# Kernel tuning notes

Hardware: AMD Instinct MI355X
Metric: run time of the kernel (lower is better)

Reference implementation:

```python
import jax, jax.numpy as jnp
import numpy as np

B, M, D, H = 2, 2048, 1024, 16
DH = D // H            # 64 head dim
FF = 2624              # GeGLU intermediate size
EPS = 1e-5
ROPE_BASE = 10000.0


def _layernorm(x, g, b):
    mu = jnp.mean(x, axis=-1, keepdims=True)
    var = jnp.mean(jnp.square(x - mu), axis=-1, keepdims=True)
    return (x - mu) * jax.lax.rsqrt(var + EPS) * g + b


def _rope_cos_sin(m, dh):
    # HF-style: inv_freq over even dims; only first dh/2 entries are used by apply_rope
    inv_freq = 1.0 / (ROPE_BASE ** (jnp.arange(0, dh, 2, dtype=jnp.float32) / dh))  # [dh/2]
    ang = jnp.arange(m, dtype=jnp.float32)[:, None] * inv_freq[None, :]             # [M, dh/2]
    return jnp.cos(ang), jnp.sin(ang)


def _apply_rope(x, c, s):
    # x: [B,H,M,dh]; c,s: [M,dh/2] broadcast over B,H. Half-split (non-interleaved) rotation.
    x1, x2 = jnp.split(x, 2, axis=-1)
    return jnp.concatenate([x1 * c - x2 * s, x1 * s + x2 * c], axis=-1)


def setup_inputs() -> dict:
    key = jax.random.key(0)
    ks = jax.random.split(key, 6)
    w = lambda k, shape: (jax.random.normal(k, shape, jnp.float32) * 0.02)
    return {
        "hidden_states": jax.random.normal(ks[0], (B, M, D), jnp.float32),
        "attention_mask": jnp.ones((B, M), jnp.int32),
        "ln1_g": jnp.ones((D,), jnp.float32),
        "ln1_b": jnp.zeros((D,), jnp.float32),
        "Wqkv_w": w(ks[1], (3 * D, D)),
        "Wqkv_b": jnp.zeros((3 * D,), jnp.float32),
        "Wo_w": w(ks[2], (D, D)),
        "ln2_g": jnp.ones((D,), jnp.float32),
        "ln2_b": jnp.zeros((D,), jnp.float32),
        "Wi_w": w(ks[3], (2 * FF, D)),
        "Wmlp_o_w": w(ks[4], (D, FF)),
    }


def reference(hidden_states, attention_mask, ln1_g, ln1_b, Wqkv_w, Wqkv_b, Wo_w,
              ln2_g, ln2_b, Wi_w, Wmlp_o_w):
    x = hidden_states                                    # [B,M,D]
    xn = _layernorm(x, ln1_g, ln1_b)
    qkv = xn @ Wqkv_w.T + Wqkv_b                         # [B,M,3D]
    qkv = qkv.reshape(B, M, 3, H, DH).transpose(0, 3, 1, 2, 4)  # [B,H,M,3,dh]
    q, k, v = qkv[..., 0, :], qkv[..., 1, :], qkv[..., 2, :]    # each [B,H,M,dh]

    c, s = _rope_cos_sin(M, DH)                          # [M, dh/2]
    q = _apply_rope(q, c, s)
    k = _apply_rope(k, c, s)

    scale = 1.0 / np.sqrt(DH)
    scores = jnp.einsum("bhmd,bhnd->bhmn", q, k) * scale  # [B,H,M,M]
    keep = (attention_mask > 0)[:, None, None, :]         # [B,1,1,M] padding mask on keys
    scores = jnp.where(keep, scores, -jnp.inf)
    p = jax.nn.softmax(scores, axis=-1)
    o = jnp.einsum("bhmn,bhnd->bhmd", p, v)               # [B,H,M,dh]

    attn_out = o.transpose(0, 2, 1, 3).reshape(B, M, D)
    x = x + attn_out @ Wo_w.T

    # ModernBERT GeGLU MLP: input, gate = Wi(x).chunk(2); Wo(gelu(input) * gate)
    xn2 = _layernorm(x, ln2_g, ln2_b)
    hg = xn2 @ Wi_w.T                                     # [B,M,2*FF]
    h_in, h_gate = jnp.split(hg, 2, axis=-1)
    x = x + (jax.nn.gelu(h_in) * h_gate) @ Wmlp_o_w.T
    return x
```

## Files before the change

kernel.cpp:

```cpp
#include <hip/hip_runtime.h>
#include <cstdint>
#include <cstddef>

using u16 = unsigned short;
using u32 = uint32_t;

typedef __attribute__((ext_vector_type(8))) short short8;
typedef __attribute__((ext_vector_type(4))) float floatx4;
typedef __attribute__((ext_vector_type(4))) unsigned int uintx4;

#define DEVFN static __device__ __forceinline__

#define QSCALE 0.18033688011112042f

DEVFN u16 f2bf(float f) {
  u32 u = __float_as_uint(f);
  return (u16)((u + 0x7fffu + ((u >> 16) & 1u)) >> 16);
}

DEVFN float b2f(u16 u) { return __uint_as_float(((u32)u) << 16); }

DEVFN u32 pkbf(float lo, float hi) {
  return __builtin_amdgcn_perm(__float_as_uint(hi) + 0x8000u,
                               __float_as_uint(lo) + 0x8000u, 0x07060302u);
}

DEVFN void async_load16(const void* g, const void* lds) {
  __builtin_amdgcn_global_load_lds(
      (const __attribute__((address_space(1))) u32*)(uintptr_t)g,
      (__attribute__((address_space(3))) u32*)(u32)(uintptr_t)lds,
      16, 0, 0);
}

DEVFN void cvt4(const float* __restrict__ src, u16* __restrict__ dst, int i) {
  const float4 v = ((const float4*)src)[i];
  ushort4 o;
  o.x = f2bf(v.x); o.y = f2bf(v.y); o.z = f2bf(v.z); o.w = f2bf(v.w);
  ((ushort4*)dst)[i] = o;
}

__global__ __launch_bounds__(256)
void prep_k(const float* __restrict__ Wqkv, const float* __restrict__ Wo,
            const float* __restrict__ Wi, const float* __restrict__ Wmlp,
            const float* __restrict__ hidden, const float* __restrict__ ln1g,
            const float* __restrict__ ln1b,
            u16* __restrict__ wqkv_bf, u16* __restrict__ wo_bf,
            u16* __restrict__ wi_bf, u16* __restrict__ wmlp_bf,
            float* __restrict__ ct, float* __restrict__ st, u16* __restrict__ xn) {
  const int bid = blockIdx.x;
  const int tid = threadIdx.x;
  __shared__ float red[8];
  if (bid < 256) {
    const int i = bid * 256 + tid;
    const int m = i >> 5, f = i & 31;
    const float inv = exp2f((float)f * -0.41524101186092025f);
    const float ang = (float)m * inv;
    ct[i] = cosf(ang);
    st[i] = sinf(ang);
  } else if (bid < 3328) {
    cvt4(Wqkv, wqkv_bf, (bid - 256) * 256 + tid);
  } else if (bid < 4352) {
    cvt4(Wo, wo_bf, (bid - 3328) * 256 + tid);
  } else if (bid < 9600) {
    const int i = (bid - 4352) * 256 + tid;
    const int i4 = i * 4;
    const int p = i4 >> 10, kc = i4 & 1023;
    const int g = p >> 5, c = p & 31;
    const int srow = (c < 16) ? (g * 16 + c) : (2624 + g * 16 + (c - 16));
    const float4 v = *(const float4*)(Wi + (size_t)srow * 1024 + kc);
    ushort4 o;
    o.x = f2bf(v.x); o.y = f2bf(v.y); o.z = f2bf(v.z); o.w = f2bf(v.w);
    ((ushort4*)wi_bf)[i] = o;
  } else if (bid < 12224) {
    cvt4(Wmlp, wmlp_bf, (bid - 9600) * 256 + tid);
  } else {
    const int row = bid - 12224;
    const float4 v = ((const float4*)(hidden + (size_t)row * 1024))[tid];
    float s = v.x + v.y + v.z + v.w;
    float ss = v.x * v.x + v.y * v.y + v.z * v.z + v.w * v.w;
#pragma unroll
    for (int d = 32; d > 0; d >>= 1) {
      s += __shfl_xor(s, d);
      ss += __shfl_xor(ss, d);
    }
    const int wave = tid >> 6;
    if ((tid & 63) == 0) { red[wave] = s; red[4 + wave] = ss; }
    __syncthreads();
    s = red[0] + red[1] + red[2] + red[3];
    ss = red[4] + red[5] + red[6] + red[7];
    const float mu = s * (1.f / 1024.f);
    const float var = ss * (1.f / 1024.f) - mu * mu;
    const float rr = rsqrtf(var + 1e-5f);
    const float4 gv = ((const float4*)ln1g)[tid];
    const float4 bv = ((const float4*)ln1b)[tid];
    u16* orow = xn + (size_t)row * 1024 + tid * 4;
    orow[0] = f2bf((v.x - mu) * rr * gv.x + bv.x);
    orow[1] = f2bf((v.y - mu) * rr * gv.y + bv.y);
    orow[2] = f2bf((v.z - mu) * rr * gv.z + bv.z);
    orow[3] = f2bf((v.w - mu) * rr * gv.w + bv.w);
  }
}

__global__ __launch_bounds__(256)
void red_ln_k(const float* __restrict__ resid, const u16* __restrict__ p0,
              const u16* __restrict__ p1, const u16* __restrict__ p2,
              const float* __restrict__ g, const float* __restrict__ bb,
              float* __restrict__ outx, u16* __restrict__ outn) {
  const int row = blockIdx.x;
  const int tid = threadIdx.x;
  const size_t base = (size_t)row * 1024;
  const float4 h = ((const float4*)(resid + base))[tid];
  const ushort4 a = ((const ushort4*)(p0 + base))[tid];
  const ushort4 c = ((const ushort4*)(p1 + base))[tid];
  const ushort4 d = ((const ushort4*)(p2 + base))[tid];
  float4 v;
  v.x = h.x + b2f(a.x) + b2f(c.x) + b2f(d.x);
  v.y = h.y + b2f(a.y) + b2f(c.y) + b2f(d.y);
  v.z = h.z + b2f(a.z) + b2f(c.z) + b2f(d.z);
  v.w = h.w + b2f(a.w) + b2f(c.w) + b2f(d.w);
  float s = v.x + v.y + v.z + v.w;
  float ss = v.x * v.x + v.y * v.y + v.z * v.z + v.w * v.w;
#pragma unroll
  for (int dd = 32; dd > 0; dd >>= 1) {
    s += __shfl_xor(s, dd);
    ss += __shfl_xor(ss, dd);
  }
  __shared__ float red[8];
  const int wave = tid >> 6;
  if ((tid & 63) == 0) { red[wave] = s; red[4 + wave] = ss; }
  __syncthreads();
  s = red[0] + red[1] + red[2] + red[3];
  ss = red[4] + red[5] + red[6] + red[7];
  const float mu = s * (1.f / 1024.f);
  const float var = ss * (1.f / 1024.f) - mu * mu;
  const float rr = rsqrtf(var + 1e-5f);
  ((float4*)(outx + base))[tid] = v;
  const float4 gv = ((const float4*)g)[tid];
  const float4 bv = ((const float4*)bb)[tid];
  u16* orow = outn + base + tid * 4;
  orow[0] = f2bf((v.x - mu) * rr * gv.x + bv.x);
  orow[1] = f2bf((v.y - mu) * rr * gv.y + bv.y);
  orow[2] = f2bf((v.z - mu) * rr * gv.z + bv.z);
  orow[3] = f2bf((v.w - mu) * rr * gv.w + bv.w);
}

__global__ void red_add_k(float* __restrict__ out, const u16* __restrict__ p0,
                          const u16* __restrict__ p1, const u16* __restrict__ p2,
                          const u16* __restrict__ p3) {
  const int i = blockIdx.x * 256 + threadIdx.x;
  float4 v = ((const float4*)out)[i];
  const ushort4 a = ((const ushort4*)p0)[i];
  const ushort4 c = ((const ushort4*)p1)[i];
  const ushort4 d = ((const ushort4*)p2)[i];
  const ushort4 e = ((const ushort4*)p3)[i];
  v.x += b2f(a.x) + b2f(c.x) + b2f(d.x) + b2f(e.x);
  v.y += b2f(a.y) + b2f(c.y) + b2f(d.y) + b2f(e.y);
  v.z += b2f(a.z) + b2f(c.z) + b2f(d.z) + b2f(e.z);
  v.w += b2f(a.w) + b2f(c.w) + b2f(d.w) + b2f(e.w);
  ((float4*)out)[i] = v;
}

__global__ __launch_bounds__(256)
void red_att_k(u16* __restrict__ att, const u16* __restrict__ p0,
               const float* __restrict__ li0, const float* __restrict__ li1) {
  const int i = blockIdx.x * 256 + threadIdx.x;
  const int i4 = i * 4;
  const int row = i4 >> 10;
  const int col = i4 & 1023;
  const int b = row >> 11, m = row & 2047;
  const int h = col >> 6;
  const int bhm = (b * 16 + h) * 2048 + m;
  const float rl = 1.f / (li0[bhm] + li1[bhm]);
  const ushort4 a = ((const ushort4*)p0)[i];
  const ushort4 c = ((const ushort4*)att)[i];
  ushort4 o;
  o.x = f2bf((b2f(a.x) + b2f(c.x)) * rl);
  o.y = f2bf((b2f(a.y) + b2f(c.y)) * rl);
  o.z = f2bf((b2f(a.z) + b2f(c.z)) * rl);
  o.w = f2bf((b2f(a.w) + b2f(c.w)) * rl);
  ((ushort4*)att)[i] = o;
}

DEVFN void swizzle_tile(int NT, int& tn, int& tm) {
  const int tpx = gridDim.x >> 3;
  const int p = blockIdx.x;
  const int lid = (p & 7) * tpx + (p >> 3);
  const int band = lid / (8 * NT);
  const int rem = lid - band * 8 * NT;
  tn = (rem >> 3) * 128;
  tm = (band * 8 + (rem & 7)) * 128;
}

struct EpiArgs {
  const float* bias;
  u16* q; u16* kk; u16* vt;
  u16* outbf;
  const float* ct; const float* st;
};

template <int EPI>
__global__ __launch_bounds__(256, 3)
void gemm_k(const u16* __restrict__ A, const u16* __restrict__ B, int K, int NT,
            EpiArgs ea) {
  __shared__ __align__(16) u16 sA[128 * 32];
  __shared__ __align__(16) u16 sB[128 * 32];
  int tn, tm;
  swizzle_tile(NT, tn, tm);
  const int tid = threadIdx.x;
  const int wave = tid >> 6, lane = tid & 63;
  const int quad = lane >> 4, l15 = lane & 15;
  const int wm = (wave >> 1) * 64, wn = (wave & 1) * 64;

  floatx4 acc[4][4];
#pragma unroll
  for (int i = 0; i < 4; ++i)
#pragma unroll
    for (int j = 0; j < 4; ++j) acc[i][j] = (floatx4){0.f, 0.f, 0.f, 0.f};

  const int srow = lane >> 2;
  const int skc = (lane & 3) * 8;
  const u16* sAr = sA + (wm + l15) * 32 + quad * 8;
  const u16* sBr = sB + (wn + l15) * 32 + quad * 8;

  for (int k0 = 0; k0 < K; k0 += 32) {
#pragma unroll
    for (int j = 0; j < 2; ++j) {
      const int q = wave * 2 + j;
      const int row = q * 16 + srow;
      async_load16(A + (size_t)(tm + row) * K + (k0 + skc), (const char*)sA + q * 1024);
      async_load16(B + (size_t)(tn + row) * K + (k0 + skc), (const char*)sB + q * 1024);
    }
    __syncthreads();
    short8 af[4], bfr[4];
#pragma unroll
    for (int t = 0; t < 4; ++t) af[t] = *(const short8*)(sAr + t * 512);
#pragma unroll
    for (int t = 0; t < 4; ++t) bfr[t] = *(const short8*)(sBr + t * 512);
#pragma unroll
    for (int ti = 0; ti < 4; ++ti)
#pragma unroll
      for (int tj = 0; tj < 4; ++tj)
        acc[ti][tj] = __builtin_amdgcn_mfma_f32_16x16x32_bf16(af[ti], bfr[tj], acc[ti][tj], 0, 0, 0);
    __syncthreads();
  }

  if constexpr (EPI == 0) {
    const int col0 = tn + wn;
    const int t = col0 >> 10;
    const int h = (col0 & 1023) >> 6;
    if (t == 2) {
#pragma unroll
      for (int ti = 0; ti < 4; ++ti)
#pragma unroll
        for (int r = 0; r < 4; ++r) {
          const int row = tm + wm + ti * 16 + quad * 4 + r;
          const int b = row >> 11, m = row & 2047;
          const int mp = (m & ~31) | ((m & 12) << 1) | ((m & 16) >> 2) | (m & 3);
#pragma unroll
          for (int tj = 0; tj < 4; ++tj) {
            const int dh = tj * 16 + l15;
            const float v = acc[ti][tj][r] + ea.bias[col0 + dh];
            ea.vt[((size_t)((b * 16 + h) * 64 + dh)) * 2048 + mp] = f2bf(v);
          }
        }
    } else {
      u16* dst = (t == 0) ? ea.q : ea.kk;
      const float qs = (t == 0) ? QSCALE : 1.f;
#pragma unroll
      for (int ti = 0; ti < 4; ++ti)
#pragma unroll
        for (int r = 0; r < 4; ++r) {
          const int row = tm + wm + ti * 16 + quad * 4 + r;
          const int b = row >> 11, m = row & 2047;
          u16* drow = dst + ((size_t)(b * 16 + h) * 2048 + m) * 64;
#pragma unroll
          for (int tj = 0; tj < 2; ++tj) {
            const int i = tj * 16 + l15;
            const float x1 = acc[ti][tj][r] + ea.bias[col0 + i];
            const float x2 = acc[ti][tj + 2][r] + ea.bias[col0 + 32 + i];
            const float cs = ea.ct[m * 32 + i];
            const float sn = ea.st[m * 32 + i];
            drow[i] = f2bf((x1 * cs - x2 * sn) * qs);
            drow[32 + i] = f2bf((x1 * sn + x2 * cs) * qs);
          }
        }
    }
  } else {
#pragma unroll
    for (int ti = 0; ti < 4; ++ti)
#pragma unroll
      for (int r = 0; r < 4; ++r) {
        const int row = tm + wm + ti * 16 + quad * 4 + r;
#pragma unroll
        for (int u = 0; u < 2; ++u) {
          const float hin = acc[ti][2 * u][r];
          const float hg = acc[ti][2 * u + 1][r];
          const int a = (((tn + wn) >> 5) + u) * 16 + l15;
          const float t2 = hin + 0.044715f * hin * hin * hin;
          const float e = __builtin_amdgcn_exp2f(t2 * -2.302114768f);
          const float gl = hin * __builtin_amdgcn_rcpf(1.f + e);
          ea.outbf[(size_t)row * 2624 + a] = f2bf(gl * hg);
        }
      }
  }
}

__global__ __launch_bounds__(256, 3)
void gemm_sk4(const u16* __restrict__ A, const u16* __restrict__ B, int K, int NT,
              int kps1, int zsw, int kps2,
              u16* __restrict__ p0, u16* __restrict__ p1,
              u16* __restrict__ p2, u16* __restrict__ p3) {
  __shared__ __align__(16) u16 sA[128 * 32];
  __shared__ __align__(16) u16 sB[128 * 32];
  int tn, tm;
  swizzle_tile(NT, tn, tm);
  const int z = blockIdx.y;
  int kofs, kps;
  if (z < zsw) { kofs = z * kps1; kps = kps1; }
  else { kofs = zsw * kps1 + (z - zsw) * kps2; kps = kps2; }
  const int tid = threadIdx.x;
  const int wave = tid >> 6, lane = tid & 63;
  const int quad = lane >> 4, l15 = lane & 15;
  const int wm = (wave >> 1) * 64, wn = (wave & 1) * 64;

  floatx4 acc[4][4];
#pragma unroll
  for (int i = 0; i < 4; ++i)
#pragma unroll
    for (int j = 0; j < 4; ++j) acc[i][j] = (floatx4){0.f, 0.f, 0.f, 0.f};

  const int srow = lane >> 2;
  const int skc = (lane & 3) * 8;
  const u16* sAr = sA + (wm + l15) * 32 + quad * 8;
  const u16* sBr = sB + (wn + l15) * 32 + quad * 8;

  for (int k0 = 0; k0 < kps; k0 += 32) {
    const int kk = kofs + k0;
#pragma unroll
    for (int j = 0; j < 2; ++j) {
      const int q = wave * 2 + j;
      const int row = q * 16 + srow;
      async_load16(A + (size_t)(tm + row) * K + (kk + skc), (const char*)sA + q * 1024);
      async_load16(B + (size_t)(tn + row) * K + (kk + skc), (const char*)sB + q * 1024);
    }
    __syncthreads();
    short8 af[4], bfr[4];
#pragma unroll
    for (int t = 0; t < 4; ++t) af[t] = *(const short8*)(sAr + t * 512);
#pragma unroll
    for (int t = 0; t < 4; ++t) bfr[t] = *(const short8*)(sBr + t * 512);
#pragma unroll
    for (int ti = 0; ti < 4; ++ti)
#pragma unroll
      for (int tj = 0; tj < 4; ++tj)
        acc[ti][tj] = __builtin_amdgcn_mfma_f32_16x16x32_bf16(af[ti], bfr[tj], acc[ti][tj], 0, 0, 0);
    __syncthreads();
  }

  u16* part = (z == 0) ? p0 : (z == 1) ? p1 : (z == 2) ? p2 : p3;
#pragma unroll
  for (int ti = 0; ti < 4; ++ti)
#pragma unroll
    for (int r = 0; r < 4; ++r) {
      const int row = tm + wm + ti * 16 + quad * 4 + r;
#pragma unroll
      for (int tj = 0; tj < 4; ++tj)
        part[(size_t)row * 1024 + tn + wn + tj * 16 + l15] = f2bf(acc[ti][tj][r]);
    }
}

DEVFN void attn_stage64(const u16* __restrict__ kg, const u16* __restrict__ vtg,
                        size_t bhk, size_t bhv, int key0, int wave, int lane,
                        const u16* sK, const u16* sV) {
#pragma unroll
  for (int j = 0; j < 4; ++j) {
    const int qi = wave * 4 + j;
    if (qi < 8) {
      async_load16(kg + bhk + (size_t)(key0 + lane) * 64 + qi * 8,
                   (const char*)sK + qi * 1024);
    } else {
      const int vi = qi - 8;
      const int c = vi >> 2, kc = vi & 3;
      async_load16(vtg + bhv + (size_t)lane * 2048 + key0 + c * 32 + kc * 8,
                   (const char*)sV + vi * 1024);
    }
  }
}

__global__ __launch_bounds__(256, 3)
void attn_k(const u16* __restrict__ qg, const u16* __restrict__ kg,
            const u16* __restrict__ vtg, const int* __restrict__ mask,
            u16* __restrict__ p0g, u16* __restrict__ p1g,
            float* __restrict__ li0, float* __restrict__ li1) {
  __shared__ __align__(16) u16 sKV[2][8192];
  const int L = blockIdx.x;
  const int xcd = L & 7, idx = L >> 3;
  const int bh = (xcd << 2) | (idx >> 5);
  const int local = idx & 31;
  const int q0 = (local >> 1) * 128;
  const int z = local & 1;
  const int keyBase = z << 10;
  const int b = bh >> 4, h = bh & 15;
  const int tid = threadIdx.x;
  const int wave = tid >> 6, lane = tid & 63;
  const int quad = lane >> 4, l15 = lane & 15;
  const size_t bhk = (size_t)bh * 2048 * 64;
  const size_t bhv = (size_t)bh * 64 * 2048;

  u32 avbits = 0;
#pragma unroll
  for (int kt = 0; kt < 16; ++kt) {
    const bool ok = mask[b * 2048 + keyBase + kt * 64 + lane] > 0;
    if (__all(ok)) avbits |= (1u << kt);
  }

  short8 aq[2][2];
#pragma unroll
  for (int g = 0; g < 2; ++g) {
    const u16* qptr = qg + ((size_t)bh * 2048 + q0 + wave * 32 + g * 16 + l15) * 64 + quad * 8;
    aq[g][0] = *(const short8*)qptr;
    aq[g][1] = *(const short8*)(qptr + 32);
  }

  floatx4 o[2][4];
#pragma unroll
  for (int g = 0; g < 2; ++g)
#pragma unroll
    for (int t = 0; t < 4; ++t) o[g][t] = (floatx4){0.f, 0.f, 0.f, 0.f};
  float li[2] = {0.f, 0.f};
  const floatx4 z4 = {0.f, 0.f, 0.f, 0.f};

  attn_stage64(kg, vtg, bhk, bhv, keyBase, wave, lane, sKV[0], sKV[0] + 4096);
  __syncthreads();

  int buf = 0;
  for (int kt = 0; kt < 16; ++kt) {
    const u16* sK = sKV[buf];
    const u16* sV = sKV[buf] + 4096;
    const int key0 = keyBase + kt * 64;
    if (kt < 15) {
      attn_stage64(kg, vtg, bhk, bhv, key0 + 64, wave, lane,
                   sKV[buf ^ 1], sKV[buf ^ 1] + 4096);
    }
    const bool allv = (avbits >> kt) & 1u;

    short8 pa[2][2];
#pragma unroll
    for (int g = 0; g < 2; ++g) {
      floatx4 sacc[4];
      __builtin_amdgcn_s_setprio(1);
#pragma unroll
      for (int tj = 0; tj < 4; ++tj) {
        const short8 b0 = *(const short8*)(sK + quad * 512 + (tj * 16 + l15) * 8);
        const short8 b1 = *(const short8*)(sK + (4 + quad) * 512 + (tj * 16 + l15) * 8);
        sacc[tj] = __builtin_amdgcn_mfma_f32_16x16x32_bf16(b0, aq[g][0], z4, 0, 0, 0);
        sacc[tj] = __builtin_amdgcn_mfma_f32_16x16x32_bf16(b1, aq[g][1], sacc[tj], 0, 0, 0);
      }
      __builtin_amdgcn_s_setprio(0);

      if (allv) {
        float sum = li[g];
#pragma unroll
        for (int tj = 0; tj < 4; ++tj)
#pragma unroll
          for (int r = 0; r < 4; ++r) {
            const float p = __builtin_amdgcn_exp2f(sacc[tj][r]);
            sacc[tj][r] = p;
            sum += p;
          }
        li[g] = sum;
      } else {
        float sum = li[g];
#pragma unroll
        for (int tj = 0; tj < 4; ++tj)
#pragma unroll
          for (int r = 0; r < 4; ++r) {
            const int key = key0 + tj * 16 + quad * 4 + r;
            const float mb = (mask[b * 2048 + key] > 0) ? 0.f : -1e30f;
            const float p = __builtin_amdgcn_exp2f(sacc[tj][r] + mb);
            sacc[tj][r] = p;
            sum += p;
          }
        li[g] = sum;
      }

#pragma unroll
      for (int c = 0; c < 2; ++c) {
        uintx4 w;
        w.x = pkbf(sacc[2 * c][0], sacc[2 * c][1]);
        w.y = pkbf(sacc[2 * c][2], sacc[2 * c][3]);
        w.z = pkbf(sacc[2 * c + 1][0], sacc[2 * c + 1][1]);
        w.w = pkbf(sacc[2 * c + 1][2], sacc[2 * c + 1][3]);
        pa[g][c] = __builtin_bit_cast(short8, w);
      }
    }

#pragma unroll
    for (int c = 0; c < 2; ++c) {
      __builtin_amdgcn_s_setprio(1);
#pragma unroll
      for (int tj2 = 0; tj2 < 4; ++tj2) {
        const short8 bv = *(const short8*)(sV + (c * 4 + quad) * 512 + (tj2 * 16 + l15) * 8);
        o[0][tj2] = __builtin_amdgcn_mfma_f32_16x16x32_bf16(pa[0][c], bv, o[0][tj2], 0, 0, 0);
        o[1][tj2] = __builtin_amdgcn_mfma_f32_16x16x32_bf16(pa[1][c], bv, o[1][tj2], 0, 0, 0);
      }
      __builtin_amdgcn_s_setprio(0);
    }
    __syncthreads();
    buf ^= 1;
  }

#pragma unroll
  for (int g = 0; g < 2; ++g) {
    float s = li[g];
    s += __shfl_xor(s, 16);
    s += __shfl_xor(s, 32);
    li[g] = s;
  }

  u16* pz = z ? p1g : p0g;
  float* lz = z ? li1 : li0;
  if (lane < 16) {
#pragma unroll
    for (int g = 0; g < 2; ++g)
      lz[(size_t)bh * 2048 + q0 + wave * 32 + g * 16 + l15] = li[g];
  }

#pragma unroll
  for (int g = 0; g < 2; ++g)
#pragma unroll
    for (int tj = 0; tj < 4; ++tj)
#pragma unroll
      for (int r = 0; r < 4; ++r) {
        const int m = q0 + wave * 32 + g * 16 + quad * 4 + r;
        pz[((size_t)b * 2048 + m) * 1024 + h * 64 + tj * 16 + l15] = f2bf(o[g][tj][r]);
      }
}

static const size_t OFF_WQKV = 0;
static const size_t OFF_WO   = 6291456;
static const size_t OFF_WI   = 8388608;
static const size_t OFF_WMLP = 19136512;
static const size_t OFF_XN   = 24510464;
static const size_t OFF_Q    = 32899072;
static const size_t OFF_K    = 41287680;
static const size_t OFF_VT   = 49676288;
static const size_t OFF_ATT  = 58064896;
static const size_t OFF_ROPE = OFF_ATT;
static const size_t WS_NEED  = 66453504;

extern "C" void kernel_launch(void* const* d_in, const int* in_sizes, int n_in,
                              void* d_out, int out_size, void* d_ws, size_t ws_size,
                              hipStream_t stream) {
  (void)in_sizes; (void)n_in; (void)out_size;
  if (ws_size < WS_NEED) return;

  const float* hidden = (const float*)d_in[0];
  const int*   mask   = (const int*)d_in[1];
  const float* ln1g   = (const float*)d_in[2];
  const float* ln1b   = (const float*)d_in[3];
  const float* Wqkv   = (const float*)d_in[4];
  const float* Wqkvb  = (const float*)d_in[5];
  const float* Wo     = (const float*)d_in[6];
  const float* ln2g   = (const float*)d_in[7];
  const float* ln2b   = (const float*)d_in[8];
  const float* Wi     = (const float*)d_in[9];
  const float* Wmlp   = (const float*)d_in[10];
  float* out = (float*)d_out;
  char* ws = (char*)d_ws;

  u16* wqkv_bf = (u16*)(ws + OFF_WQKV);
  u16* wo_bf   = (u16*)(ws + OFF_WO);
  u16* wi_bf   = (u16*)(ws + OFF_WI);
  u16* wmlp_bf = (u16*)(ws + OFF_WMLP);
  u16* xn      = (u16*)(ws + OFF_XN);
  u16* qb      = (u16*)(ws + OFF_Q);
  u16* kb      = (u16*)(ws + OFF_K);
  u16* vtb     = (u16*)(ws + OFF_VT);
  u16* att     = (u16*)(ws + OFF_ATT);
  u16* act     = (u16*)(ws + OFF_Q);
  float* ct    = (float*)(ws + OFF_ROPE);
  float* st    = (float*)(ws + OFF_ROPE + 262144);
  u16* ap0     = (u16*)(ws + OFF_XN);
  u16* ap1     = (u16*)(ws + OFF_ATT);
  float* li0   = (float*)(ws + OFF_WQKV);
  float* li1   = (float*)(ws + OFF_WQKV + 262144);
  u16* wp0     = (u16*)(ws + OFF_Q);
  u16* wp1     = (u16*)(ws + OFF_K);
  u16* wp2     = (u16*)(ws + OFF_VT);
  u16* mp0     = (u16*)(ws + OFF_XN);
  u16* mp1     = (u16*)(ws + OFF_ATT);
  u16* mp2     = (u16*)(ws + OFF_WI);
  u16* mp3     = (u16*)(ws + OFF_WQKV);

  prep_k<<<16320, 256, 0, stream>>>(Wqkv, Wo, Wi, Wmlp, hidden, ln1g, ln1b,
                                    wqkv_bf, wo_bf, wi_bf, wmlp_bf, ct, st, xn);

  EpiArgs e1 = {Wqkvb, qb, kb, vtb, nullptr, ct, st};
  gemm_k<0><<<768, 256, 0, stream>>>(xn, wqkv_bf, 1024, 24, e1);

  attn_k<<<dim3(1024), 256, 0, stream>>>(qb, kb, vtb, mask, ap0, ap1, li0, li1);
  red_att_k<<<4096, 256, 0, stream>>>(att, ap0, li0, li1);

  gemm_sk4<<<dim3(256, 3), 256, 0, stream>>>(att, wo_bf, 1024, 8, 352, 2, 320,
                                             wp0, wp1, wp2, wp2);
  red_ln_k<<<4096, 256, 0, stream>>>(hidden, wp0, wp1, wp2, ln2g, ln2b, out, xn);

  EpiArgs e3 = {nullptr, nullptr, nullptr, nullptr, act, nullptr, nullptr};
  gemm_k<2><<<1312, 256, 0, stream>>>(xn, wi_bf, 1024, 41, e3);

  gemm_sk4<<<dim3(256, 4), 256, 0, stream>>>(act, wmlp_bf, 2624, 8, 672, 2, 640,
                                             mp0, mp1, mp2, mp3);
  red_add_k<<<4096, 256, 0, stream>>>(out, mp0, mp1, mp2, mp3);
}
```

Measured before the change: 335.4 us.

## Stage GEMM epilogues through LDS for coalesced stores; interleave attention score MFMAs

The GeGLU GEMM epilogue and the split-K partial-sum epilogue now write their bf16 tiles into the reused shared-memory buffer first. Each thread then copies contiguous 16-byte chunks to global memory, replacing scattered 2-byte stores with coalesced wide ones. The attention kernel also computes the scores for both query groups before the softmax, which loads each K fragment once for two MFMAs and exposes more independent MFMA work. The cost is extra __syncthreads barriers and LDS traffic in the epilogues, plus more live score registers in attention.

```diff
diff --git a/kernel.cpp b/kernel.cpp
--- a/kernel.cpp
+++ b/kernel.cpp
@@ -202,8 +202,9 @@
 __global__ __launch_bounds__(256, 3)
 void gemm_k(const u16* __restrict__ A, const u16* __restrict__ B, int K, int NT,
             EpiArgs ea) {
-  __shared__ __align__(16) u16 sA[128 * 32];
-  __shared__ __align__(16) u16 sB[128 * 32];
+  __shared__ __align__(16) u16 sAB[8192];
+  u16* const sA = sAB;
+  u16* const sB = sAB + 4096;
   int tn, tm;
   swizzle_tile(NT, tn, tm);
   const int tid = threadIdx.x;
@@ -286,22 +287,28 @@
         }
     }
   } else {
+    u16* eb = sAB;
 #pragma unroll
     for (int ti = 0; ti < 4; ++ti)
 #pragma unroll
       for (int r = 0; r < 4; ++r) {
-        const int row = tm + wm + ti * 16 + quad * 4 + r;
+        const int lrow = wm + ti * 16 + quad * 4 + r;
 #pragma unroll
         for (int u = 0; u < 2; ++u) {
           const float hin = acc[ti][2 * u][r];
           const float hg = acc[ti][2 * u + 1][r];
-          const int a = (((tn + wn) >> 5) + u) * 16 + l15;
           const float t2 = hin + 0.044715f * hin * hin * hin;
           const float e = __builtin_amdgcn_exp2f(t2 * -2.302114768f);
           const float gl = hin * __builtin_amdgcn_rcpf(1.f + e);
-          ea.outbf[(size_t)row * 2624 + a] = f2bf(gl * hg);
+          eb[lrow * 64 + (wn >> 1) + u * 16 + l15] = f2bf(gl * hg);
         }
       }
+    __syncthreads();
+    const int row = tid >> 1, ch = (tid & 1) * 32;
+    const short8* src = (const short8*)(eb + row * 64 + ch);
+    u16* dst = ea.outbf + (size_t)(tm + row) * 2624 + (tn >> 1) + ch;
+#pragma unroll
+    for (int j = 0; j < 4; ++j) ((short8*)dst)[j] = src[j];
   }
 }
 
@@ -310,8 +317,9 @@
               int kps1, int zsw, int kps2,
               u16* __restrict__ p0, u16* __restrict__ p1,
               u16* __restrict__ p2, u16* __restrict__ p3) {
-  __shared__ __align__(16) u16 sA[128 * 32];
-  __shared__ __align__(16) u16 sB[128 * 32];
+  __shared__ __align__(16) u16 sAB[8192];
+  u16* const sA = sAB;
+  u16* const sB = sAB + 4096;
   int tn, tm;
   swizzle_tile(NT, tn, tm);
   const int z = blockIdx.y;
@@ -358,15 +366,28 @@
   }
 
   u16* part = (z == 0) ? p0 : (z == 1) ? p1 : (z == 2) ? p2 : p3;
-#pragma unroll
-  for (int ti = 0; ti < 4; ++ti)
-#pragma unroll
-    for (int r = 0; r < 4; ++r) {
-      const int row = tm + wm + ti * 16 + quad * 4 + r;
-#pragma unroll
-      for (int tj = 0; tj < 4; ++tj)
-        part[(size_t)row * 1024 + tn + wn + tj * 16 + l15] = f2bf(acc[ti][tj][r]);
-    }
+  u16* eb = sAB;
+#pragma unroll
+  for (int p = 0; p < 2; ++p) {
+    if ((wave & 1) == p) {
+#pragma unroll
+      for (int ti = 0; ti < 4; ++ti)
+#pragma unroll
+        for (int r = 0; r < 4; ++r) {
+          const int lrow = wm + ti * 16 + quad * 4 + r;
+#pragma unroll
+          for (int tj = 0; tj < 4; ++tj)
+            eb[lrow * 64 + tj * 16 + l15] = f2bf(acc[ti][tj][r]);
+        }
+    }
+    __syncthreads();
+    const int row = tid >> 1, ch = (tid & 1) * 32;
+    const short8* src = (const short8*)(eb + row * 64 + ch);
+    u16* dst = part + (size_t)(tm + row) * 1024 + tn + p * 64 + ch;
+#pragma unroll
+    for (int j = 0; j < 4; ++j) ((short8*)dst)[j] = src[j];
+    if (p == 0) __syncthreads();
+  }
 }
 
 DEVFN void attn_stage64(const u16* __restrict__ kg, const u16* __restrict__ vtg,
@@ -445,53 +466,57 @@
     const bool allv = (avbits >> kt) & 1u;
 
     short8 pa[2][2];
-#pragma unroll
-    for (int g = 0; g < 2; ++g) {
-      floatx4 sacc[4];
+    {
+      floatx4 sc[2][4];
       __builtin_amdgcn_s_setprio(1);
 #pragma unroll
       for (int tj = 0; tj < 4; ++tj) {
         const short8 b0 = *(const short8*)(sK + quad * 512 + (tj * 16 + l15) * 8);
         const short8 b1 = *(const short8*)(sK + (4 + quad) * 512 + (tj * 16 + l15) * 8);
-        sacc[tj] = __builtin_amdgcn_mfma_f32_16x16x32_bf16(b0, aq[g][0], z4, 0, 0, 0);
-        sacc[tj] = __builtin_amdgcn_mfma_f32_16x16x32_bf16(b1, aq[g][1], sacc[tj], 0, 0, 0);
+        sc[0][tj] = __builtin_amdgcn_mfma_f32_16x16x32_bf16(b0, aq[0][0], z4, 0, 0, 0);
+        sc[0][tj] = __builtin_amdgcn_mfma_f32_16x16x32_bf16(b1, aq[0][1], sc[0][tj], 0, 0, 0);
+        sc[1][tj] = __builtin_amdgcn_mfma_f32_16x16x32_bf16(b0, aq[1][0], z4, 0, 0, 0);
+        sc[1][tj] = __builtin_amdgcn_mfma_f32_16x16x32_bf16(b1, aq[1][1], sc[1][tj], 0, 0, 0);
       }
       __builtin_amdgcn_s_setprio(0);
 
-      if (allv) {
-        float sum = li[g];
-#pragma unroll
-        for (int tj = 0; tj < 4; ++tj)
-#pragma unroll
-          for (int r = 0; r < 4; ++r) {
-            const float p = __builtin_amdgcn_exp2f(sacc[tj][r]);
-            sacc[tj][r] = p;
-            sum += p;
-          }
-        li[g] = sum;
-      } else {
-        float sum = li[g];
-#pragma unroll
-        for (int tj = 0; tj < 4; ++tj)
-#pragma unroll
-          for (int r = 0; r < 4; ++r) {
-            const int key = key0 + tj * 16 + quad * 4 + r;
-            const float mb = (mask[b * 2048 + key] > 0) ? 0.f : -1e30f;
-            const float p = __builtin_amdgcn_exp2f(sacc[tj][r] + mb);
-            sacc[tj][r] = p;
-            sum += p;
-          }
-        li[g] = sum;
-      }
-
-#pragma unroll
-      for (int c = 0; c < 2; ++c) {
-        uintx4 w;
-        w.x = pkbf(sacc[2 * c][0], sacc[2 * c][1]);
-        w.y = pkbf(sacc[2 * c][2], sacc[2 * c][3]);
-        w.z = pkbf(sacc[2 * c + 1][0], sacc[2 * c + 1][1]);
-        w.w = pkbf(sacc[2 * c + 1][2], sacc[2 * c + 1][3]);
-        pa[g][c] = __builtin_bit_cast(short8, w);
+#pragma unroll
+      for (int g = 0; g < 2; ++g) {
+        if (allv) {
+          float sum = li[g];
+#pragma unroll
+          for (int tj = 0; tj < 4; ++tj)
+#pragma unroll
+            for (int r = 0; r < 4; ++r) {
+              const float p = __builtin_amdgcn_exp2f(sc[g][tj][r]);
+              sc[g][tj][r] = p;
+              sum += p;
+            }
+          li[g] = sum;
+        } else {
+          float sum = li[g];
+#pragma unroll
+          for (int tj = 0; tj < 4; ++tj)
+#pragma unroll
+            for (int r = 0; r < 4; ++r) {
+              const int key = key0 + tj * 16 + quad * 4 + r;
+              const float mb = (mask[b * 2048 + key] > 0) ? 0.f : -1e30f;
+              const float p = __builtin_amdgcn_exp2f(sc[g][tj][r] + mb);
+              sc[g][tj][r] = p;
+              sum += p;
+            }
+          li[g] = sum;
+        }
+
+#pragma unroll
+        for (int c = 0; c < 2; ++c) {
+          uintx4 w;
+          w.x = pkbf(sc[g][2 * c][0], sc[g][2 * c][1]);
+          w.y = pkbf(sc[g][2 * c][2], sc[g][2 * c][3]);
+          w.z = pkbf(sc[g][2 * c + 1][0], sc[g][2 * c + 1][1]);
+          w.w = pkbf(sc[g][2 * c + 1][2], sc[g][2 * c + 1][3]);
+          pa[g][c] = __builtin_bit_cast(short8, w);
+        }
       }
     }
 
```

Result: slower. 354.9 us (+5.8%).

## Double-buffer LDS tiles in GEMM kernels to overlap loads with MFMA

Applied to the files above, without the earlier changes.

Both GEMM kernels (the epilogue-fused one and the split-K one) now use two LDS buffers for the A and B tiles. The first k-slice is prefetched before the loop. Each iteration then issues the async global-to-LDS load for the next slice into the other buffer while MFMAs run on the current one, and the second barrier per iteration is dropped. This is meant to hide global memory latency behind compute and cut synchronisation, at the cost of doubling LDS use per block, which could limit occupancy.

```diff
diff --git a/kernel.cpp b/kernel.cpp
--- a/kernel.cpp
+++ b/kernel.cpp
@@ -202,8 +202,8 @@
 __global__ __launch_bounds__(256, 3)
 void gemm_k(const u16* __restrict__ A, const u16* __restrict__ B, int K, int NT,
             EpiArgs ea) {
-  __shared__ __align__(16) u16 sA[128 * 32];
-  __shared__ __align__(16) u16 sB[128 * 32];
+  __shared__ __align__(16) u16 sA[2][4096];
+  __shared__ __align__(16) u16 sB[2][4096];
   int tn, tm;
   swizzle_tile(NT, tn, tm);
   const int tid = threadIdx.x;
@@ -219,18 +219,31 @@
 
   const int srow = lane >> 2;
   const int skc = (lane & 3) * 8;
-  const u16* sAr = sA + (wm + l15) * 32 + quad * 8;
-  const u16* sBr = sB + (wn + l15) * 32 + quad * 8;
-
+  const int q0i = wave * 2;
+  const int row0 = q0i * 16 + srow;
+  const int row1 = row0 + 16;
+  const size_t aoff0 = (size_t)(tm + row0) * K + skc;
+  const size_t aoff1 = (size_t)(tm + row1) * K + skc;
+  const size_t boff0 = (size_t)(tn + row0) * K + skc;
+  const size_t boff1 = (size_t)(tn + row1) * K + skc;
+
+  async_load16(A + aoff0, (const char*)sA[0] + q0i * 1024);
+  async_load16(B + boff0, (const char*)sB[0] + q0i * 1024);
+  async_load16(A + aoff1, (const char*)sA[0] + (q0i + 1) * 1024);
+  async_load16(B + boff1, (const char*)sB[0] + (q0i + 1) * 1024);
+
+  int buf = 0;
   for (int k0 = 0; k0 < K; k0 += 32) {
-#pragma unroll
-    for (int j = 0; j < 2; ++j) {
-      const int q = wave * 2 + j;
-      const int row = q * 16 + srow;
-      async_load16(A + (size_t)(tm + row) * K + (k0 + skc), (const char*)sA + q * 1024);
-      async_load16(B + (size_t)(tn + row) * K + (k0 + skc), (const char*)sB + q * 1024);
-    }
     __syncthreads();
+    if (k0 + 32 < K) {
+      const int kn = k0 + 32;
+      async_load16(A + aoff0 + kn, (const char*)sA[buf ^ 1] + q0i * 1024);
+      async_load16(B + boff0 + kn, (const char*)sB[buf ^ 1] + q0i * 1024);
+      async_load16(A + aoff1 + kn, (const char*)sA[buf ^ 1] + (q0i + 1) * 1024);
+      async_load16(B + boff1 + kn, (const char*)sB[buf ^ 1] + (q0i + 1) * 1024);
+    }
+    const u16* sAr = sA[buf] + (wm + l15) * 32 + quad * 8;
+    const u16* sBr = sB[buf] + (wn + l15) * 32 + quad * 8;
     short8 af[4], bfr[4];
 #pragma unroll
     for (int t = 0; t < 4; ++t) af[t] = *(const short8*)(sAr + t * 512);
@@ -241,7 +254,7 @@
 #pragma unroll
       for (int tj = 0; tj < 4; ++tj)
         acc[ti][tj] = __builtin_amdgcn_mfma_f32_16x16x32_bf16(af[ti], bfr[tj], acc[ti][tj], 0, 0, 0);
-    __syncthreads();
+    buf ^= 1;
   }
 
   if constexpr (EPI == 0) {
@@ -310,8 +323,8 @@
               int kps1, int zsw, int kps2,
               u16* __restrict__ p0, u16* __restrict__ p1,
               u16* __restrict__ p2, u16* __restrict__ p3) {
-  __shared__ __align__(16) u16 sA[128 * 32];
-  __shared__ __align__(16) u16 sB[128 * 32];
+  __shared__ __align__(16) u16 sA[2][4096];
+  __shared__ __align__(16) u16 sB[2][4096];
   int tn, tm;
   swizzle_tile(NT, tn, tm);
   const int z = blockIdx.y;
@@ -331,19 +344,31 @@
 
   const int srow = lane >> 2;
   const int skc = (lane & 3) * 8;
-  const u16* sAr = sA + (wm + l15) * 32 + quad * 8;
-  const u16* sBr = sB + (wn + l15) * 32 + quad * 8;
-
+  const int q0i = wave * 2;
+  const int row0 = q0i * 16 + srow;
+  const int row1 = row0 + 16;
+  const size_t aoff0 = (size_t)(tm + row0) * K + kofs + skc;
+  const size_t aoff1 = (size_t)(tm + row1) * K + kofs + skc;
+  const size_t boff0 = (size_t)(tn + row0) * K + kofs + skc;
+  const size_t boff1 = (size_t)(tn + row1) * K + kofs + skc;
+
+  async_load16(A + aoff0, (const char*)sA[0] + q0i * 1024);
+  async_load16(B + boff0, (const char*)sB[0] + q0i * 1024);
+  async_load16(A + aoff1, (const char*)sA[0] + (q0i + 1) * 1024);
+  async_load16(B + boff1, (const char*)sB[0] + (q0i + 1) * 1024);
+
+  int buf = 0;
   for (int k0 = 0; k0 < kps; k0 += 32) {
-    const int kk = kofs + k0;
-#pragma unroll
-    for (int j = 0; j < 2; ++j) {
-      const int q = wave * 2 + j;
-      const int row = q * 16 + srow;
-      async_load16(A + (size_t)(tm + row) * K + (kk + skc), (const char*)sA + q * 1024);
-      async_load16(B + (size_t)(tn + row) * K + (kk + skc), (const char*)sB + q * 1024);
-    }
     __syncthreads();
+    if (k0 + 32 < kps) {
+      const int kn = k0 + 32;
+      async_load16(A + aoff0 + kn, (const char*)sA[buf ^ 1] + q0i * 1024);
+      async_load16(B + boff0 + kn, (const char*)sB[buf ^ 1] + q0i * 1024);
+      async_load16(A + aoff1 + kn, (const char*)sA[buf ^ 1] + (q0i + 1) * 1024);
+      async_load16(B + boff1 + kn, (const char*)sB[buf ^ 1] + (q0i + 1) * 1024);
+    }
+    const u16* sAr = sA[buf] + (wm + l15) * 32 + quad * 8;
+    const u16* sBr = sB[buf] + (wn + l15) * 32 + quad * 8;
     short8 af[4], bfr[4];
 #pragma unroll
     for (int t = 0; t < 4; ++t) af[t] = *(const short8*)(sAr + t * 512);
@@ -354,7 +379,7 @@
 #pragma unroll
       for (int tj = 0; tj < 4; ++tj)
         acc[ti][tj] = __builtin_amdgcn_mfma_f32_16x16x32_bf16(af[ti], bfr[tj], acc[ti][tj], 0, 0, 0);
-    __syncthreads();
+    buf ^= 1;
   }
 
   u16* part = (z == 0) ? p0 : (z == 1) ? p1 : (z == 2) ? p2 : p3;
```

After: 332.1 us. About the same (-1.0%).
